# Optimization experiments

Measured on AMD Instinct MI355X. Metric: run time of the kernel, lower is better.

The kernel has to match this reference:

```python
import jax, jax.numpy as jnp
import numpy as np

# graph layout constants
B = 64        # number of graphs
NPG = 512     # nodes per graph
N = B * NPG   # total nodes
DEG = 16      # avg degree
E = N * DEG   # total edges
F_IN = 256
H, C = 4, 64  # heads, per-head dim
K = NPG // 2  # topk pooling keeps ratio=0.5 per graph


def setup_inputs() -> dict:
    key = jax.random.key(0)
    ks = jax.random.split(key, 8)
    x = jax.random.normal(ks[0], (N, F_IN), dtype=jnp.float32)
    # within-graph random edges (src -> dst), contiguous node ids per graph
    offs = jnp.repeat(jnp.arange(B, dtype=jnp.int64) * NPG, NPG * DEG)
    src = offs + jax.random.randint(ks[1], (E,), 0, NPG)
    dst = offs + jax.random.randint(ks[2], (E,), 0, NPG)
    edge_index = jnp.stack([src, dst]).astype(jnp.int64)
    W = jax.random.normal(ks[3], (F_IN, H, C), dtype=jnp.float32) / np.sqrt(F_IN)
    att_src = jax.random.normal(ks[4], (H, C), dtype=jnp.float32) / np.sqrt(C)
    att_dst = jax.random.normal(ks[5], (H, C), dtype=jnp.float32) / np.sqrt(C)
    bias = jnp.zeros((H * C,), dtype=jnp.float32)
    bn_gamma = jnp.ones((H * C,), dtype=jnp.float32)
    bn_beta = jnp.zeros((H * C,), dtype=jnp.float32)
    pool_weight = jax.random.normal(ks[6], (H * C,), dtype=jnp.float32) / np.sqrt(H * C)
    return {"x": x, "edge_index": edge_index, "W": W, "att_src": att_src,
            "att_dst": att_dst, "bias": bias, "bn_gamma": bn_gamma,
            "bn_beta": bn_beta, "pool_weight": pool_weight}


def reference(x, edge_index, W, att_src, att_dst, bias, bn_gamma, bn_beta, pool_weight):
    n = x.shape[0]
    # --- GATConv ---
    h = jnp.einsum('nf,fhc->nhc', x, W)                 # [N,H,C]
    a_src = jnp.sum(h * att_src, axis=-1)               # [N,H]
    a_dst = jnp.sum(h * att_dst, axis=-1)               # [N,H]
    loops = jnp.arange(n, dtype=edge_index.dtype)        # add_self_loops=True default
    src = jnp.concatenate([edge_index[0], loops])
    dst = jnp.concatenate([edge_index[1], loops])
    e = jax.nn.leaky_relu(a_src[src] + a_dst[dst], 0.2)  # [E+N,H]
    # scatter-softmax over edges grouped by destination node
    emax = jax.ops.segment_max(e, dst, num_segments=n)
    ex = jnp.exp(e - emax[dst])
    den = jax.ops.segment_sum(ex, dst, num_segments=n)
    alpha = ex / (den[dst] + 1e-16)                      # [E+N,H]
    msg = alpha[:, :, None] * h[src]                     # [E+N,H,C]
    out = jax.ops.segment_sum(msg, dst, num_segments=n)  # [N,H,C]
    feat = out.reshape(n, H * C) + bias                  # concat heads
    # --- ReLU + BatchNorm (batch stats, training mode) ---
    feat = jax.nn.relu(feat)
    mean = jnp.mean(feat, axis=0)
    var = jnp.var(feat, axis=0)
    feat = (feat - mean) * jax.lax.rsqrt(var + 1e-5) * bn_gamma + bn_beta
    # --- TopKPooling (score = x.w/||w||, keep top ratio per graph, gate by tanh) ---
    score = feat @ pool_weight / jnp.linalg.norm(pool_weight)  # [N]
    top_s, top_i = jax.lax.top_k(score.reshape(B, NPG), K)     # [B,K]
    fg = feat.reshape(B, NPG, H * C)
    sel = jnp.take_along_axis(fg, top_i[:, :, None], axis=1)    # [B,K,HC]
    pooled = sel * jnp.tanh(top_s)[:, :, None]
    return pooled.reshape(B * K, H * C)
```

## Files before the change

kernel.cpp:

```cpp
#include <hip/hip_runtime.h>
#include <math.h>

#define N_NODES 32768
#define NPG 512
#define NGRAPH 64
#define KKEEP 256
#define CAP 64

typedef __attribute__((ext_vector_type(8))) short short8;
typedef __attribute__((ext_vector_type(4))) float f32x4;

__device__ __forceinline__ unsigned short f2bf(float v) {
  unsigned u = __builtin_bit_cast(unsigned, v);
  u = (u + 0x7FFFu + ((u >> 16) & 1u)) >> 16;
  return (unsigned short)u;
}
__device__ __forceinline__ float bf2f(unsigned short u) {
  unsigned v = ((unsigned)u) << 16;
  return __builtin_bit_cast(float, v);
}

__global__ __launch_bounds__(256) void k_hist_conv(
    const int* __restrict__ ei, int E, int* __restrict__ cnt,
    unsigned short* __restrict__ nbr,
    const float* __restrict__ W,
    unsigned short* __restrict__ wth, unsigned short* __restrict__ wtl,
    unsigned short* __restrict__ wtll) {
  const int t = threadIdx.x;
  if (blockIdx.x < 2048) {
    int e = blockIdx.x * 256 + t;
    if (e < E) {
      int s = ei[e];
      int d = ei[E + e];
      int slot = atomicAdd(&cnt[d], 1);
      if (slot < CAP) nbr[(size_t)d * CAP + slot] = (unsigned short)(s & (NPG - 1));
    }
  } else {
    int bw = blockIdx.x - 2048;
    int n = bw * 4 + (t >> 6);
    int k = (t & 63) * 4;
    unsigned short hb[4], lb[4], qb[4];
#pragma unroll
    for (int j = 0; j < 4; j++) {
      float v = W[(size_t)(k + j) * 256 + n];
      unsigned short hh = f2bf(v);
      float e1 = v - bf2f(hh);
      unsigned short ll = f2bf(e1);
      float e2 = e1 - bf2f(ll);
      hb[j] = hh; lb[j] = ll; qb[j] = f2bf(e2);
    }
    *(uint2*)&wth[(size_t)n * 256 + k] = *(uint2*)&hb[0];
    *(uint2*)&wtl[(size_t)n * 256 + k] = *(uint2*)&lb[0];
    *(uint2*)&wtll[(size_t)n * 256 + k] = *(uint2*)&qb[0];
  }
}

__global__ __launch_bounds__(256) void k_gemm(
    const float* __restrict__ x,
    const unsigned short* __restrict__ wth, const unsigned short* __restrict__ wtl,
    const unsigned short* __restrict__ wtll,
    const float* __restrict__ attS, const float* __restrict__ attD,
    float* __restrict__ h, float* __restrict__ a_src, float* __restrict__ a_dst) {
  __shared__ unsigned short lds[24576];
  const int t = threadIdx.x;
  const int bid = blockIdx.x;
  const int mb = (bid & 7) * 32 + (bid >> 4);
  const int nh = (bid >> 3) & 1;
  const int row0 = mb * 128;
  const int wid = t >> 6, lane = t & 63;
  const int q = lane >> 4, ln = lane & 15;
  const int wm = (wid >> 1) * 64, wn = (wid & 1) * 64;
  f32x4 acc[4][4] = {};

  for (int kc = 0; kc < 8; kc++) {
    const int k0 = kc * 32;
#pragma unroll
    for (int i = 0; i < 2; i++) {
      int c = i * 256 + t;
      int r = c >> 2, cq = c & 3;
      size_t ga = (size_t)(row0 + r) * 256 + k0 + cq * 8;
      float4 f0 = *(const float4*)&x[ga];
      float4 f1 = *(const float4*)&x[ga + 4];
      float ff[8] = {f0.x, f0.y, f0.z, f0.w, f1.x, f1.y, f1.z, f1.w};
      unsigned short hs[8], ls[8], qs[8];
#pragma unroll
      for (int j = 0; j < 8; j++) {
        unsigned short hh = f2bf(ff[j]);
        float e1 = ff[j] - bf2f(hh);
        unsigned short ll = f2bf(e1);
        float e2 = e1 - bf2f(ll);
        hs[j] = hh; ls[j] = ll; qs[j] = f2bf(e2);
      }
      *(uint4*)&lds[((0 * 4 + cq) * 128 + r) * 8] = *(uint4*)&hs[0];
      *(uint4*)&lds[((1 * 4 + cq) * 128 + r) * 8] = *(uint4*)&ls[0];
      *(uint4*)&lds[((2 * 4 + cq) * 128 + r) * 8] = *(uint4*)&qs[0];
      size_t gb = (size_t)(nh * 128 + r) * 256 + k0 + cq * 8;
      *(uint4*)&lds[12288 + ((0 * 4 + cq) * 128 + r) * 8] = *(const uint4*)&wth[gb];
      *(uint4*)&lds[12288 + ((1 * 4 + cq) * 128 + r) * 8] = *(const uint4*)&wtl[gb];
      *(uint4*)&lds[12288 + ((2 * 4 + cq) * 128 + r) * 8] = *(const uint4*)&wtll[gb];
    }
    __syncthreads();
    short8 ah[4], al[4], aq[4];
#pragma unroll
    for (int mt = 0; mt < 4; mt++) {
      int r = wm + mt * 16 + ln;
      ah[mt] = *(const short8*)&lds[((0 * 4 + q) * 128 + r) * 8];
      al[mt] = *(const short8*)&lds[((1 * 4 + q) * 128 + r) * 8];
      aq[mt] = *(const short8*)&lds[((2 * 4 + q) * 128 + r) * 8];
    }
#pragma unroll
    for (int nt = 0; nt < 4; nt++) {
      int r = wn + nt * 16 + ln;
      short8 bh = *(const short8*)&lds[12288 + ((0 * 4 + q) * 128 + r) * 8];
      short8 bl = *(const short8*)&lds[12288 + ((1 * 4 + q) * 128 + r) * 8];
      short8 bq = *(const short8*)&lds[12288 + ((2 * 4 + q) * 128 + r) * 8];
#pragma unroll
      for (int mt = 0; mt < 4; mt++) {
        acc[mt][nt] = __builtin_amdgcn_mfma_f32_16x16x32_bf16(ah[mt], bh, acc[mt][nt], 0, 0, 0);
        acc[mt][nt] = __builtin_amdgcn_mfma_f32_16x16x32_bf16(ah[mt], bl, acc[mt][nt], 0, 0, 0);
        acc[mt][nt] = __builtin_amdgcn_mfma_f32_16x16x32_bf16(al[mt], bh, acc[mt][nt], 0, 0, 0);
        acc[mt][nt] = __builtin_amdgcn_mfma_f32_16x16x32_bf16(ah[mt], bq, acc[mt][nt], 0, 0, 0);
        acc[mt][nt] = __builtin_amdgcn_mfma_f32_16x16x32_bf16(al[mt], bl, acc[mt][nt], 0, 0, 0);
        acc[mt][nt] = __builtin_amdgcn_mfma_f32_16x16x32_bf16(aq[mt], bh, acc[mt][nt], 0, 0, 0);
      }
    }
    __syncthreads();
  }
  const int head = nh * 2 + (wid & 1);
  float sA[4], sD[4];
#pragma unroll
  for (int nt = 0; nt < 4; nt++) {
    int n = nh * 128 + wn + nt * 16 + ln;
    sA[nt] = attS[n];
    sD[nt] = attD[n];
  }
  float2* epi = (float2*)lds;
#pragma unroll
  for (int mt = 0; mt < 4; mt++) {
#pragma unroll
    for (int reg = 0; reg < 4; reg++) {
      int m = row0 + wm + mt * 16 + q * 4 + reg;
      float ps = 0.f, pd = 0.f;
#pragma unroll
      for (int nt = 0; nt < 4; nt++) {
        float v = acc[mt][nt][reg];
        h[(size_t)m * 256 + nh * 128 + wn + nt * 16 + ln] = v;
        ps = fmaf(v, sA[nt], ps);
        pd = fmaf(v, sD[nt], pd);
      }
      epi[(((wid * 4 + q) * 16) + mt * 4 + reg) * 18 + ln] = make_float2(ps, pd);
    }
  }
  __syncthreads();
  {
    const int q2 = lane >> 4, rr = lane & 15;
    const int base = (((wid * 4 + q2) * 16) + rr) * 18;
    float ps = 0.f, pd = 0.f;
#pragma unroll
    for (int i = 0; i < 16; i++) {
      float2 v = epi[base + i];
      ps += v.x;
      pd += v.y;
    }
    int m = row0 + wm + (rr >> 2) * 16 + q2 * 4 + (rr & 3);
    a_src[m * 4 + head] = ps;
    a_dst[m * 4 + head] = pd;
  }
}

__global__ __launch_bounds__(256) void k_agg(
    const float* __restrict__ h, const float* __restrict__ a_src,
    const float* __restrict__ a_dst, const int* __restrict__ cnt,
    const unsigned short* __restrict__ nbr, const float* __restrict__ bias,
    float* __restrict__ feat) {
  __shared__ float p_lds[4][68][4];
  __shared__ int s_lds[4][68];
  const int wv = threadIdx.x >> 6;
  const int lane = threadIdx.x & 63;
  int nb = (blockIdx.x & 7) * (N_NODES / 4 / 8) + (blockIdx.x >> 3);
  const int node = nb * 4 + wv;
  const int head = lane >> 4;
  const int li = lane & 15;
  const int c0 = lane * 4;
  const int base = node & ~(NPG - 1);
  const float ad = a_dst[node * 4 + head];
  int n = cnt[node];
  if (n > CAP) n = CAP;
  float e_reg[5];
  int srcs[5];
  int nit = 0;
  float m = -1e30f;
  for (int j = li; j <= n; j += 16) {
    int s = (j < n) ? base + (int)nbr[(size_t)node * CAP + j] : node;
    float e = a_src[s * 4 + head] + ad;
    e = (e > 0.f) ? e : 0.2f * e;
    srcs[nit] = s;
    e_reg[nit++] = e;
    m = fmaxf(m, e);
  }
#pragma unroll
  for (int d = 1; d < 16; d <<= 1) m = fmaxf(m, __shfl_xor(m, d, 16));
  float l = 0.f;
  for (int i = 0; i < nit; i++) {
    int j = li + i * 16;
    float p = __expf(e_reg[i] - m);
    l += p;
    p_lds[wv][j][head] = p;
    if (head == 0) s_lds[wv][j] = srcs[i];
  }
#pragma unroll
  for (int d = 1; d < 16; d <<= 1) l += __shfl_xor(l, d, 16);
  const float linv = 1.f / (l + 1e-16f);
  __builtin_amdgcn_s_waitcnt(0);
  float4 acc0 = make_float4(0.f, 0.f, 0.f, 0.f);
  float4 acc1 = make_float4(0.f, 0.f, 0.f, 0.f);
  int j = 0;
  for (; j + 1 <= n; j += 2) {
    float p0 = p_lds[wv][j][head];
    float p1 = p_lds[wv][j + 1][head];
    int s0 = s_lds[wv][j];
    int s1 = s_lds[wv][j + 1];
    float4 h0 = *(const float4*)&h[(size_t)s0 * 256 + c0];
    float4 h1 = *(const float4*)&h[(size_t)s1 * 256 + c0];
    acc0.x = fmaf(p0, h0.x, acc0.x); acc1.x = fmaf(p1, h1.x, acc1.x);
    acc0.y = fmaf(p0, h0.y, acc0.y); acc1.y = fmaf(p1, h1.y, acc1.y);
    acc0.z = fmaf(p0, h0.z, acc0.z); acc1.z = fmaf(p1, h1.z, acc1.z);
    acc0.w = fmaf(p0, h0.w, acc0.w); acc1.w = fmaf(p1, h1.w, acc1.w);
  }
  if (j <= n) {
    float p0 = p_lds[wv][j][head];
    int s0 = s_lds[wv][j];
    float4 h0 = *(const float4*)&h[(size_t)s0 * 256 + c0];
    acc0.x = fmaf(p0, h0.x, acc0.x);
    acc0.y = fmaf(p0, h0.y, acc0.y);
    acc0.z = fmaf(p0, h0.z, acc0.z);
    acc0.w = fmaf(p0, h0.w, acc0.w);
  }
  const float4 b4 = *(const float4*)&bias[c0];
  float4 o;
  o.x = fmaxf(fmaf(acc0.x + acc1.x, linv, b4.x), 0.f);
  o.y = fmaxf(fmaf(acc0.y + acc1.y, linv, b4.y), 0.f);
  o.z = fmaxf(fmaf(acc0.z + acc1.z, linv, b4.z), 0.f);
  o.w = fmaxf(fmaf(acc0.w + acc1.w, linv, b4.w), 0.f);
  *(float4*)&feat[(size_t)node * 256 + c0] = o;
}

__global__ __launch_bounds__(256) void k_bn_partial(const float* __restrict__ feat,
                                                    double* __restrict__ psum,
                                                    double* __restrict__ psq) {
  const int c = threadIdx.x;
  const int r0 = blockIdx.x * 128;
  double s = 0.0, q = 0.0;
  for (int i = 0; i < 128; i++) {
    double v = (double)feat[(size_t)(r0 + i) * 256 + c];
    s += v;
    q += v * v;
  }
  psum[blockIdx.x * 256 + c] = s;
  psq[blockIdx.x * 256 + c] = q;
}

__global__ __launch_bounds__(1024) void k_bn_final(
    const double* __restrict__ psum, const double* __restrict__ psq,
    const float* __restrict__ gam, const float* __restrict__ bet,
    const float* __restrict__ pw, float* __restrict__ cA, float* __restrict__ cB,
    float* __restrict__ sv) {
  __shared__ double reds[4][256];
  __shared__ double redq[4][256];
  __shared__ double wsq[256];
  __shared__ double sb[256];
  const int t = threadIdx.x;
  const int c = t & 255, sl = t >> 8;
  double s = 0.0, q = 0.0;
  for (int i = sl * 64; i < sl * 64 + 64; i++) {
    s += psum[i * 256 + c];
    q += psq[i * 256 + c];
  }
  reds[sl][c] = s;
  redq[sl][c] = q;
  if (sl == 0) {
    double w = (double)pw[c];
    wsq[c] = w * w;
  }
  __syncthreads();
  if (t == 0) {
    double nn = 0.0;
    for (int i = 0; i < 256; i++) nn += wsq[i];
    wsq[0] = sqrt(nn);
  }
  __syncthreads();
  if (sl == 0) {
    s = reds[0][c] + reds[1][c] + reds[2][c] + reds[3][c];
    q = redq[0][c] + redq[1][c] + redq[2][c] + redq[3][c];
    double mean = s / (double)N_NODES;
    double var = q / (double)N_NODES - mean * mean;
    double a = (double)gam[c] / sqrt(var + 1e-5);
    double cb = (double)bet[c] - mean * a;
    cA[c] = (float)a;
    cB[c] = (float)cb;
    double pwnv = (double)pw[c] / wsq[0];
    sv[c] = (float)(a * pwnv);
    sb[c] = cb * pwnv;
  }
  __syncthreads();
  if (t == 0) {
    double s0 = 0.0;
    for (int i = 0; i < 256; i++) s0 += sb[i];
    sv[256] = (float)s0;
  }
}

__global__ __launch_bounds__(256) void k_score(
    const float* __restrict__ feat, const float* __restrict__ sv,
    float* __restrict__ score) {
  const int lane = threadIdx.x & 63;
  const int node = blockIdx.x * 4 + (threadIdx.x >> 6);
  const int c0 = lane * 4;
  float4 f = *(const float4*)&feat[(size_t)node * 256 + c0];
  float4 w = *(const float4*)&sv[c0];
  float p = f.x * w.x + f.y * w.y + f.z * w.z + f.w * w.w;
#pragma unroll
  for (int d = 1; d < 64; d <<= 1) p += __shfl_xor(p, d, 64);
  if (lane == 0) score[node] = p + sv[256];
}

__global__ __launch_bounds__(256) void k_topk(
    const float* __restrict__ score, const float* __restrict__ feat,
    const float* __restrict__ cA, const float* __restrict__ cB,
    float* __restrict__ out) {
  __shared__ float ss[NPG];
  __shared__ int rnk[64];
  __shared__ float gt[64];
  const int g = blockIdx.x >> 3;
  const int part = blockIdx.x & 7;
  const int t = threadIdx.x;
  ss[t] = score[g * NPG + t];
  ss[t + 256] = score[g * NPG + t + 256];
  __syncthreads();
  const int ln = t & 3;
  const int ndl = part * 64 + (t >> 2);
  const float s = ss[ndl];
  int rank = 0;
  for (int j = ln * 128; j < ln * 128 + 128; j++) {
    float sj = ss[j];
    rank += (sj > s || (sj == s && j < ndl)) ? 1 : 0;
  }
  rank += __shfl_xor(rank, 1);
  rank += __shfl_xor(rank, 2);
  if (ln == 0) {
    rnk[t >> 2] = rank;
    gt[t >> 2] = tanhf(s);
  }
  __syncthreads();
  for (int idx = t; idx < 64 * 64; idx += 256) {
    int r = idx >> 6;
    int rank2 = rnk[r];
    if (rank2 < KKEEP) {
      int c4 = (idx & 63) * 4;
      int node = g * NPG + part * 64 + r;
      float4 f = *(const float4*)&feat[(size_t)node * 256 + c4];
      float4 a = *(const float4*)&cA[c4];
      float4 b = *(const float4*)&cB[c4];
      float tg = gt[r];
      float4 o;
      o.x = fmaf(f.x, a.x, b.x) * tg;
      o.y = fmaf(f.y, a.y, b.y) * tg;
      o.z = fmaf(f.z, a.z, b.z) * tg;
      o.w = fmaf(f.w, a.w, b.w) * tg;
      *(float4*)&out[(size_t)(g * KKEEP + rank2) * 256 + c4] = o;
    }
  }
}

extern "C" void kernel_launch(void* const* d_in, const int* in_sizes, int n_in,
                              void* d_out, int out_size, void* d_ws, size_t ws_size,
                              hipStream_t stream) {
  const float* x    = (const float*)d_in[0];
  const int*   ei   = (const int*)d_in[1];
  const float* W    = (const float*)d_in[2];
  const float* attS = (const float*)d_in[3];
  const float* attD = (const float*)d_in[4];
  const float* bias = (const float*)d_in[5];
  const float* gam  = (const float*)d_in[6];
  const float* bet  = (const float*)d_in[7];
  const float* pw   = (const float*)d_in[8];
  float* out = (float*)d_out;
  const int E = in_sizes[1] / 2;

  char* p = (char*)d_ws;
  float* h     = (float*)p; p += (size_t)N_NODES * 256 * 4;
  float* feat  = (float*)p; p += (size_t)N_NODES * 256 * 4;
  float* a_src = (float*)p; p += (size_t)N_NODES * 4 * 4;
  float* a_dst = (float*)p; p += (size_t)N_NODES * 4 * 4;
  float* score = (float*)p; p += (size_t)N_NODES * 4;
  double* psum = (double*)p; p += (size_t)256 * 256 * 8;
  double* psq  = (double*)p; p += (size_t)256 * 256 * 8;
  float* cA    = (float*)p; p += 256 * 4;
  float* cB    = (float*)p; p += 256 * 4;
  float* sv    = (float*)p; p += 260 * 4;
  unsigned short* wth  = (unsigned short*)p; p += (size_t)256 * 256 * 2;
  unsigned short* wtl  = (unsigned short*)p; p += (size_t)256 * 256 * 2;
  unsigned short* wtll = (unsigned short*)p; p += (size_t)256 * 256 * 2;
  int* cnt     = (int*)p;   p += (size_t)N_NODES * 4;
  unsigned short* nbr = (unsigned short*)p; p += (size_t)N_NODES * CAP * 2;

  hipMemsetAsync(cnt, 0, (size_t)N_NODES * 4, stream);
  k_hist_conv<<<2112, 256, 0, stream>>>(ei, E, cnt, nbr, W, wth, wtl, wtll);
  k_gemm<<<512, 256, 0, stream>>>(x, wth, wtl, wtll, attS, attD, h, a_src, a_dst);
  k_agg<<<N_NODES / 4, 256, 0, stream>>>(h, a_src, a_dst, cnt, nbr, bias, feat);
  k_bn_partial<<<256, 256, 0, stream>>>(feat, psum, psq);
  k_bn_final<<<1, 1024, 0, stream>>>(psum, psq, gam, bet, pw, cA, cB, sv);
  k_score<<<N_NODES / 4, 256, 0, stream>>>(feat, sv, score);
  k_topk<<<NGRAPH * 8, 256, 0, stream>>>(score, feat, cA, cB, out);
}
```

Baseline: 215.7 us.

## Pre-split x into bf16 triplets in prep kernel and async-load GEMM tiles to LDS

```diff
diff --git a/kernel.cpp b/kernel.cpp
--- a/kernel.cpp
+++ b/kernel.cpp
@@ -20,12 +20,21 @@
   return __builtin_bit_cast(float, v);
 }
 
+__device__ __forceinline__ void async_cp16(unsigned short* l, const unsigned short* g) {
+  __builtin_amdgcn_global_load_lds(
+      (const __attribute__((address_space(1))) unsigned int*)g,
+      (__attribute__((address_space(3))) unsigned int*)l, 16, 0, 0);
+}
+
 __global__ __launch_bounds__(256) void k_hist_conv(
     const int* __restrict__ ei, int E, int* __restrict__ cnt,
     unsigned short* __restrict__ nbr,
     const float* __restrict__ W,
     unsigned short* __restrict__ wth, unsigned short* __restrict__ wtl,
-    unsigned short* __restrict__ wtll) {
+    unsigned short* __restrict__ wtll,
+    const float* __restrict__ x,
+    unsigned short* __restrict__ xsh, unsigned short* __restrict__ xsl,
+    unsigned short* __restrict__ xsq) {
   const int t = threadIdx.x;
   if (blockIdx.x < 2048) {
     int e = blockIdx.x * 256 + t;
@@ -35,7 +44,7 @@
       int slot = atomicAdd(&cnt[d], 1);
       if (slot < CAP) nbr[(size_t)d * CAP + slot] = (unsigned short)(s & (NPG - 1));
     }
-  } else {
+  } else if (blockIdx.x < 2112) {
     int bw = blockIdx.x - 2048;
     int n = bw * 4 + (t >> 6);
     int k = (t & 63) * 4;
@@ -52,11 +61,32 @@
     *(uint2*)&wth[(size_t)n * 256 + k] = *(uint2*)&hb[0];
     *(uint2*)&wtl[(size_t)n * 256 + k] = *(uint2*)&lb[0];
     *(uint2*)&wtll[(size_t)n * 256 + k] = *(uint2*)&qb[0];
+  } else {
+    int b2 = blockIdx.x - 2112;
+    int row = b2 * 8 + (t >> 5);
+    int o = t & 31;
+    size_t off = (size_t)row * 256 + o * 8;
+    float4 f0 = *(const float4*)&x[off];
+    float4 f1 = *(const float4*)&x[off + 4];
+    float ff[8] = {f0.x, f0.y, f0.z, f0.w, f1.x, f1.y, f1.z, f1.w};
+    unsigned short hs[8], ls[8], qs[8];
+#pragma unroll
+    for (int j = 0; j < 8; j++) {
+      unsigned short hh = f2bf(ff[j]);
+      float e1 = ff[j] - bf2f(hh);
+      unsigned short ll = f2bf(e1);
+      float e2 = e1 - bf2f(ll);
+      hs[j] = hh; ls[j] = ll; qs[j] = f2bf(e2);
+    }
+    *(uint4*)&xsh[off] = *(uint4*)&hs[0];
+    *(uint4*)&xsl[off] = *(uint4*)&ls[0];
+    *(uint4*)&xsq[off] = *(uint4*)&qs[0];
   }
 }
 
 __global__ __launch_bounds__(256) void k_gemm(
-    const float* __restrict__ x,
+    const unsigned short* __restrict__ xsh, const unsigned short* __restrict__ xsl,
+    const unsigned short* __restrict__ xsq,
     const unsigned short* __restrict__ wth, const unsigned short* __restrict__ wtl,
     const unsigned short* __restrict__ wtll,
     const float* __restrict__ attS, const float* __restrict__ attD,
@@ -76,28 +106,16 @@
     const int k0 = kc * 32;
 #pragma unroll
     for (int i = 0; i < 2; i++) {
-      int c = i * 256 + t;
-      int r = c >> 2, cq = c & 3;
+      int u = i * 256 + t;
+      int cq = u >> 7, r = u & 127;
       size_t ga = (size_t)(row0 + r) * 256 + k0 + cq * 8;
-      float4 f0 = *(const float4*)&x[ga];
-      float4 f1 = *(const float4*)&x[ga + 4];
-      float ff[8] = {f0.x, f0.y, f0.z, f0.w, f1.x, f1.y, f1.z, f1.w};
-      unsigned short hs[8], ls[8], qs[8];
-#pragma unroll
-      for (int j = 0; j < 8; j++) {
-        unsigned short hh = f2bf(ff[j]);
-        float e1 = ff[j] - bf2f(hh);
-        unsigned short ll = f2bf(e1);
-        float e2 = e1 - bf2f(ll);
-        hs[j] = hh; ls[j] = ll; qs[j] = f2bf(e2);
-      }
-      *(uint4*)&lds[((0 * 4 + cq) * 128 + r) * 8] = *(uint4*)&hs[0];
-      *(uint4*)&lds[((1 * 4 + cq) * 128 + r) * 8] = *(uint4*)&ls[0];
-      *(uint4*)&lds[((2 * 4 + cq) * 128 + r) * 8] = *(uint4*)&qs[0];
+      async_cp16(&lds[0 * 4096 + u * 8], &xsh[ga]);
+      async_cp16(&lds[1 * 4096 + u * 8], &xsl[ga]);
+      async_cp16(&lds[2 * 4096 + u * 8], &xsq[ga]);
       size_t gb = (size_t)(nh * 128 + r) * 256 + k0 + cq * 8;
-      *(uint4*)&lds[12288 + ((0 * 4 + cq) * 128 + r) * 8] = *(const uint4*)&wth[gb];
-      *(uint4*)&lds[12288 + ((1 * 4 + cq) * 128 + r) * 8] = *(const uint4*)&wtl[gb];
-      *(uint4*)&lds[12288 + ((2 * 4 + cq) * 128 + r) * 8] = *(const uint4*)&wtll[gb];
+      async_cp16(&lds[12288 + 0 * 4096 + u * 8], &wth[gb]);
+      async_cp16(&lds[12288 + 1 * 4096 + u * 8], &wtl[gb]);
+      async_cp16(&lds[12288 + 2 * 4096 + u * 8], &wtll[gb]);
     }
     __syncthreads();
     short8 ah[4], al[4], aq[4];
@@ -403,10 +421,15 @@
   unsigned short* wtll = (unsigned short*)p; p += (size_t)256 * 256 * 2;
   int* cnt     = (int*)p;   p += (size_t)N_NODES * 4;
   unsigned short* nbr = (unsigned short*)p; p += (size_t)N_NODES * CAP * 2;
+  unsigned short* xsh = (unsigned short*)p; p += (size_t)N_NODES * 256 * 2;
+  unsigned short* xsl = (unsigned short*)p; p += (size_t)N_NODES * 256 * 2;
+  unsigned short* xsq = (unsigned short*)p; p += (size_t)N_NODES * 256 * 2;
 
   hipMemsetAsync(cnt, 0, (size_t)N_NODES * 4, stream);
-  k_hist_conv<<<2112, 256, 0, stream>>>(ei, E, cnt, nbr, W, wth, wtl, wtll);
-  k_gemm<<<512, 256, 0, stream>>>(x, wth, wtl, wtll, attS, attD, h, a_src, a_dst);
+  k_hist_conv<<<6208, 256, 0, stream>>>(ei, E, cnt, nbr, W, wth, wtl, wtll,
+                                        x, xsh, xsl, xsq);
+  k_gemm<<<512, 256, 0, stream>>>(xsh, xsl, xsq, wth, wtl, wtll, attS, attD,
+                                  h, a_src, a_dst);
   k_agg<<<N_NODES / 4, 256, 0, stream>>>(h, a_src, a_dst, cnt, nbr, bias, feat);
   k_bn_partial<<<256, 256, 0, stream>>>(feat, psum, psq);
   k_bn_final<<<1, 1024, 0, stream>>>(psum, psq, gam, bet, pw, cA, cB, sv);
```

Measured after the change: 235.8 us. 9.3% more time.

## Fuse edge histogram into GEMM launch, async-load B tiles, pad A LDS stride

Applied to the files above, without the earlier changes.

```diff
diff --git a/kernel.cpp b/kernel.cpp
--- a/kernel.cpp
+++ b/kernel.cpp
@@ -20,50 +20,57 @@
   return __builtin_bit_cast(float, v);
 }
 
-__global__ __launch_bounds__(256) void k_hist_conv(
-    const int* __restrict__ ei, int E, int* __restrict__ cnt,
-    unsigned short* __restrict__ nbr,
+__device__ __forceinline__ void async_cp16(unsigned short* l, const unsigned short* g) {
+  __builtin_amdgcn_global_load_lds(
+      (const __attribute__((address_space(1))) unsigned int*)g,
+      (__attribute__((address_space(3))) unsigned int*)l, 16, 0, 0);
+}
+
+__global__ __launch_bounds__(256) void k_conv(
     const float* __restrict__ W,
     unsigned short* __restrict__ wth, unsigned short* __restrict__ wtl,
     unsigned short* __restrict__ wtll) {
   const int t = threadIdx.x;
-  if (blockIdx.x < 2048) {
-    int e = blockIdx.x * 256 + t;
+  int n = blockIdx.x * 4 + (t >> 6);
+  int k = (t & 63) * 4;
+  unsigned short hb[4], lb[4], qb[4];
+#pragma unroll
+  for (int j = 0; j < 4; j++) {
+    float v = W[(size_t)(k + j) * 256 + n];
+    unsigned short hh = f2bf(v);
+    float e1 = v - bf2f(hh);
+    unsigned short ll = f2bf(e1);
+    float e2 = e1 - bf2f(ll);
+    hb[j] = hh; lb[j] = ll; qb[j] = f2bf(e2);
+  }
+  *(uint2*)&wth[(size_t)n * 256 + k] = *(uint2*)&hb[0];
+  *(uint2*)&wtl[(size_t)n * 256 + k] = *(uint2*)&lb[0];
+  *(uint2*)&wtll[(size_t)n * 256 + k] = *(uint2*)&qb[0];
+}
+
+#define A_STR 129
+#define B_BASE 12376
+__global__ __launch_bounds__(256) void k_gemm_hist(
+    const float* __restrict__ x,
+    const unsigned short* __restrict__ wth, const unsigned short* __restrict__ wtl,
+    const unsigned short* __restrict__ wtll,
+    const float* __restrict__ attS, const float* __restrict__ attD,
+    float* __restrict__ h, float* __restrict__ a_src, float* __restrict__ a_dst,
+    const int* __restrict__ ei, int E, int* __restrict__ cnt,
+    unsigned short* __restrict__ nbr) {
+  __shared__ unsigned short lds[24664];
+  const int t = threadIdx.x;
+  const int bid = blockIdx.x;
+  if (bid >= 512) {
+    int e = (bid - 512) * 256 + t;
     if (e < E) {
       int s = ei[e];
       int d = ei[E + e];
       int slot = atomicAdd(&cnt[d], 1);
       if (slot < CAP) nbr[(size_t)d * CAP + slot] = (unsigned short)(s & (NPG - 1));
     }
-  } else {
-    int bw = blockIdx.x - 2048;
-    int n = bw * 4 + (t >> 6);
-    int k = (t & 63) * 4;
-    unsigned short hb[4], lb[4], qb[4];
-#pragma unroll
-    for (int j = 0; j < 4; j++) {
-      float v = W[(size_t)(k + j) * 256 + n];
-      unsigned short hh = f2bf(v);
-      float e1 = v - bf2f(hh);
-      unsigned short ll = f2bf(e1);
-      float e2 = e1 - bf2f(ll);
-      hb[j] = hh; lb[j] = ll; qb[j] = f2bf(e2);
-    }
-    *(uint2*)&wth[(size_t)n * 256 + k] = *(uint2*)&hb[0];
-    *(uint2*)&wtl[(size_t)n * 256 + k] = *(uint2*)&lb[0];
-    *(uint2*)&wtll[(size_t)n * 256 + k] = *(uint2*)&qb[0];
-  }
-}
-
-__global__ __launch_bounds__(256) void k_gemm(
-    const float* __restrict__ x,
-    const unsigned short* __restrict__ wth, const unsigned short* __restrict__ wtl,
-    const unsigned short* __restrict__ wtll,
-    const float* __restrict__ attS, const float* __restrict__ attD,
-    float* __restrict__ h, float* __restrict__ a_src, float* __restrict__ a_dst) {
-  __shared__ unsigned short lds[24576];
-  const int t = threadIdx.x;
-  const int bid = blockIdx.x;
+    return;
+  }
   const int mb = (bid & 7) * 32 + (bid >> 4);
   const int nh = (bid >> 3) & 1;
   const int row0 = mb * 128;
@@ -74,6 +81,15 @@
 
   for (int kc = 0; kc < 8; kc++) {
     const int k0 = kc * 32;
+#pragma unroll
+    for (int i = 0; i < 2; i++) {
+      int u = i * 256 + t;
+      int cq = u >> 7, r = u & 127;
+      size_t gb = (size_t)(nh * 128 + r) * 256 + k0 + cq * 8;
+      async_cp16(&lds[B_BASE + 0 * 4096 + u * 8], &wth[gb]);
+      async_cp16(&lds[B_BASE + 1 * 4096 + u * 8], &wtl[gb]);
+      async_cp16(&lds[B_BASE + 2 * 4096 + u * 8], &wtll[gb]);
+    }
 #pragma unroll
     for (int i = 0; i < 2; i++) {
       int c = i * 256 + t;
@@ -91,29 +107,25 @@
         float e2 = e1 - bf2f(ll);
         hs[j] = hh; ls[j] = ll; qs[j] = f2bf(e2);
       }
-      *(uint4*)&lds[((0 * 4 + cq) * 128 + r) * 8] = *(uint4*)&hs[0];
-      *(uint4*)&lds[((1 * 4 + cq) * 128 + r) * 8] = *(uint4*)&ls[0];
-      *(uint4*)&lds[((2 * 4 + cq) * 128 + r) * 8] = *(uint4*)&qs[0];
-      size_t gb = (size_t)(nh * 128 + r) * 256 + k0 + cq * 8;
-      *(uint4*)&lds[12288 + ((0 * 4 + cq) * 128 + r) * 8] = *(const uint4*)&wth[gb];
-      *(uint4*)&lds[12288 + ((1 * 4 + cq) * 128 + r) * 8] = *(const uint4*)&wtl[gb];
-      *(uint4*)&lds[12288 + ((2 * 4 + cq) * 128 + r) * 8] = *(const uint4*)&wtll[gb];
+      *(uint4*)&lds[((0 * 4 + cq) * A_STR + r) * 8] = *(uint4*)&hs[0];
+      *(uint4*)&lds[((1 * 4 + cq) * A_STR + r) * 8] = *(uint4*)&ls[0];
+      *(uint4*)&lds[((2 * 4 + cq) * A_STR + r) * 8] = *(uint4*)&qs[0];
     }
     __syncthreads();
     short8 ah[4], al[4], aq[4];
 #pragma unroll
     for (int mt = 0; mt < 4; mt++) {
       int r = wm + mt * 16 + ln;
-      ah[mt] = *(const short8*)&lds[((0 * 4 + q) * 128 + r) * 8];
-      al[mt] = *(const short8*)&lds[((1 * 4 + q) * 128 + r) * 8];
-      aq[mt] = *(const short8*)&lds[((2 * 4 + q) * 128 + r) * 8];
+      ah[mt] = *(const short8*)&lds[((0 * 4 + q) * A_STR + r) * 8];
+      al[mt] = *(const short8*)&lds[((1 * 4 + q) * A_STR + r) * 8];
+      aq[mt] = *(const short8*)&lds[((2 * 4 + q) * A_STR + r) * 8];
     }
 #pragma unroll
     for (int nt = 0; nt < 4; nt++) {
       int r = wn + nt * 16 + ln;
-      short8 bh = *(const short8*)&lds[12288 + ((0 * 4 + q) * 128 + r) * 8];
-      short8 bl = *(const short8*)&lds[12288 + ((1 * 4 + q) * 128 + r) * 8];
-      short8 bq = *(const short8*)&lds[12288 + ((2 * 4 + q) * 128 + r) * 8];
+      short8 bh = *(const short8*)&lds[B_BASE + 0 * 4096 + (q * 128 + r) * 8];
+      short8 bl = *(const short8*)&lds[B_BASE + 1 * 4096 + (q * 128 + r) * 8];
+      short8 bq = *(const short8*)&lds[B_BASE + 2 * 4096 + (q * 128 + r) * 8];
 #pragma unroll
       for (int mt = 0; mt < 4; mt++) {
         acc[mt][nt] = __builtin_amdgcn_mfma_f32_16x16x32_bf16(ah[mt], bh, acc[mt][nt], 0, 0, 0);
@@ -405,8 +417,9 @@
   unsigned short* nbr = (unsigned short*)p; p += (size_t)N_NODES * CAP * 2;
 
   hipMemsetAsync(cnt, 0, (size_t)N_NODES * 4, stream);
-  k_hist_conv<<<2112, 256, 0, stream>>>(ei, E, cnt, nbr, W, wth, wtl, wtll);
-  k_gemm<<<512, 256, 0, stream>>>(x, wth, wtl, wtll, attS, attD, h, a_src, a_dst);
+  k_conv<<<64, 256, 0, stream>>>(W, wth, wtl, wtll);
+  k_gemm_hist<<<2560, 256, 0, stream>>>(x, wth, wtl, wtll, attS, attD,
+                                        h, a_src, a_dst, ei, E, cnt, nbr);
   k_agg<<<N_NODES / 4, 256, 0, stream>>>(h, a_src, a_dst, cnt, nbr, bias, feat);
   k_bn_partial<<<256, 256, 0, stream>>>(feat, psum, psq);
   k_bn_final<<<1, 1024, 0, stream>>>(psum, psq, gam, bet, pw, cA, cB, sv);
```

New measurement: 207.9 us. -3.6%, faster.
